# Kernel optimization log

Measured on AMD Instinct MI355X. Metric: run time of the kernel, lower is better.

## Reference

```python
import jax, jax.numpy as jnp
import numpy as np

C = 256   # descriptor_dim
H = 4     # num_heads
D = C // H  # head_dim = 64
B, N = 8, 2048


def _conv1x1(x, w, b):
    # 1x1 Conv1d == per-position linear over channels: x [B,C,N], w [O,C], b [O]
    return jnp.einsum('oc,bcn->bon', w, x) + b[None, :, None]


def setup_inputs() -> dict:
    key = jax.random.key(0)
    ks = jax.random.split(key, 11)
    s = 1.0 / np.sqrt(C)
    return {
        'query': jax.random.normal(ks[0], (B, C, N), dtype=jnp.float32),
        'key':   jax.random.normal(ks[1], (B, C, N), dtype=jnp.float32),
        'value': jax.random.normal(ks[2], (B, C, N), dtype=jnp.float32),
        'wq': jax.random.normal(ks[3], (C, C), dtype=jnp.float32) * s,
        'bq': jax.random.normal(ks[4], (C,), dtype=jnp.float32) * s,
        'wk': jax.random.normal(ks[5], (C, C), dtype=jnp.float32) * s,
        'bk': jax.random.normal(ks[6], (C,), dtype=jnp.float32) * s,
        'wv': jax.random.normal(ks[7], (C, C), dtype=jnp.float32) * s,
        'bv': jax.random.normal(ks[8], (C,), dtype=jnp.float32) * s,
        'wm': jax.random.normal(ks[9], (C, C), dtype=jnp.float32) * s,
        'bm': jax.random.normal(ks[10], (C,), dtype=jnp.float32) * s,
    }


def reference(query, key, value, wq, bq, wk, bk, wv, bv, wm, bm):
    b = query.shape[0]
    # project then view channels as (head_dim, num_heads) -- matches torch .view order
    q = _conv1x1(query, wq, bq).reshape(b, D, H, -1)   # [B,D,H,N]
    k = _conv1x1(key,   wk, bk).reshape(b, D, H, -1)   # [B,D,H,M]
    v = _conv1x1(value, wv, bv).reshape(b, D, H, -1)   # [B,D,H,M]
    scores = jnp.einsum('bdhn,bdhm->bhnm', q, k) / (D ** 0.5)
    probs = jax.nn.softmax(scores, axis=-1)            # [B,H,N,M]
    out = jnp.einsum('bhnm,bdhm->bdhn', probs, v)      # [B,D,H,N]
    out = out.reshape(b, D * H, -1)                    # [B,C,N]
    return _conv1x1(out, wm, bm)
```

## Files before the change

### kernel.cpp

```cpp
#include <hip/hip_runtime.h>
#include <hip/hip_bf16.h>

typedef float f32x4 __attribute__((ext_vector_type(4)));
typedef float f32x16 __attribute__((ext_vector_type(16)));
typedef __bf16 bf16x8 __attribute__((ext_vector_type(8)));
typedef __bf16 bf16x4 __attribute__((ext_vector_type(4)));
typedef unsigned int uint2v __attribute__((ext_vector_type(2)));
typedef unsigned int u32;

constexpr int B_ = 8, C_ = 256, N_ = 2048, H_ = 4, D_ = 64;
constexpr int BH_ = B_ * H_;
constexpr size_t PER_ = (size_t)BH_ * N_ * D_;
constexpr float LOG2E = 1.44269504088896340736f;

static __device__ __forceinline__ float fast_exp2(float x) {
#if __has_builtin(__builtin_amdgcn_exp2f)
  return __builtin_amdgcn_exp2f(x);
#else
  return exp2f(x);
#endif
}

static __device__ __forceinline__ void* swz(void* base, int row, int cb) {
  return (char*)base + row * 128 + (cb ^ ((row & 7) << 4));
}
static __device__ __forceinline__ const void* swz(const void* base, int row, int cb) {
  return (const char*)base + row * 128 + (cb ^ ((row & 7) << 4));
}

static __device__ __forceinline__ void gload16(void* lds, const void* g) {
  __builtin_amdgcn_global_load_lds(
      (const __attribute__((address_space(1))) u32*)g,
      (__attribute__((address_space(3))) u32*)lds, 16, 0, 0);
}

struct W4 {
  const float* s0; const float* s1; const float* s2; const float* s3;
  __bf16* d0; __bf16* d1; __bf16* d2; __bf16* d3;
};

__global__ __launch_bounds__(256) void wcvt_kernel(W4 p) {
  const int m = blockIdx.y;
  const float* src = m == 0 ? p.s0 : m == 1 ? p.s1 : m == 2 ? p.s2 : p.s3;
  __bf16* dst = m == 0 ? p.d0 : m == 1 ? p.d1 : m == 2 ? p.d2 : p.d3;
  const int f = blockIdx.x * 256 + threadIdx.x;
  const int o_blk = f >> 9;
  const int ks = (f >> 6) & 7;
  const int lane = f & 63;
  const int row = o_blk * 16 + (lane & 15);
  const int kbase = ks * 32 + (lane >> 4) * 8;
  bf16x8 v;
  if (m == 3) {
    for (int e = 0; e < 8; e++) {
      const int k = kbase + e;
      const int c = ((k & 63) << 2) | (k >> 6);
      v[e] = (__bf16)src[row * 256 + c];
    }
  } else {
    const int srow = ((row & 63) << 2) | (row >> 6);
    const float* s = src + srow * 256 + kbase;
    float4 a = *(const float4*)s;
    float4 b = *(const float4*)(s + 4);
    v[0] = (__bf16)a.x; v[1] = (__bf16)a.y; v[2] = (__bf16)a.z; v[3] = (__bf16)a.w;
    v[4] = (__bf16)b.x; v[5] = (__bf16)b.y; v[6] = (__bf16)b.z; v[7] = (__bf16)b.w;
  }
  *(bf16x8*)&dst[(size_t)f * 8] = v;
}

__global__ __launch_bounds__(256) void qkv_fused_kernel(
    const float* __restrict__ xq, const float* __restrict__ xk,
    const float* __restrict__ xv, const __bf16* __restrict__ wfq,
    const __bf16* __restrict__ wfk, const __bf16* __restrict__ wfv,
    const float* __restrict__ bq, const float* __restrict__ bk,
    const float* __restrict__ bv, __bf16* __restrict__ oq,
    char* __restrict__ oksw, char* __restrict__ ovsw) {
  __shared__ __bf16 xlds[64][264];

  const int m = blockIdx.x >> 8;
  int inner = blockIdx.x & 255;
  inner = (inner & 7) * 32 + (inner >> 3);
  const int b = inner >> 5, nb = inner & 31;
  const int n0 = nb * 64;

  const float* xf = m == 0 ? xq : m == 1 ? xk : xv;
  const __bf16* wf = m == 0 ? wfq : m == 1 ? wfk : wfv;
  const float* bias = m == 0 ? bq : m == 1 ? bk : bv;
  const float scale = m == 0 ? 0.125f * LOG2E : 1.0f;

  const int t = threadIdx.x;
  {
    const int kl = t & 15;
    const int nl = (t >> 4) * 4;
    const float* src = xf + (size_t)b * C_ * N_ + n0 + nl;
    for (int kp = 0; kp < 8; kp++) {
      const int k = kp * 32 + kl * 2;
      float4 f0 = *(const float4*)(src + (size_t)k * N_);
      float4 f1 = *(const float4*)(src + (size_t)(k + 1) * N_);
      union { __bf16 h[2]; u32 u; } c0, c1, c2, c3;
      c0.h[0] = (__bf16)f0.x; c0.h[1] = (__bf16)f1.x;
      c1.h[0] = (__bf16)f0.y; c1.h[1] = (__bf16)f1.y;
      c2.h[0] = (__bf16)f0.z; c2.h[1] = (__bf16)f1.z;
      c3.h[0] = (__bf16)f0.w; c3.h[1] = (__bf16)f1.w;
      *(u32*)&xlds[nl + 0][k] = c0.u;
      *(u32*)&xlds[nl + 1][k] = c1.u;
      *(u32*)&xlds[nl + 2][k] = c2.u;
      *(u32*)&xlds[nl + 3][k] = c3.u;
    }
  }
  __syncthreads();

  const int lane = t & 63, wvv = t >> 6;
  const int wm = wvv >> 1, wn = wvv & 1;
  const int l15 = lane & 15, lg = lane >> 4;

  f32x4 acc[8][2] = {};

  for (int ks = 0; ks < 8; ks++) {
    bf16x8 bfr[2];
    for (int ni = 0; ni < 2; ni++)
      bfr[ni] = *(const bf16x8*)&xlds[wn * 32 + ni * 16 + l15][ks * 32 + lg * 8];
    for (int mi = 0; mi < 8; mi++) {
      bf16x8 af = *(const bf16x8*)&wf[(((size_t)(wm * 8 + mi) * 8 + ks) * 64 + lane) * 8];
      acc[mi][0] = __builtin_amdgcn_mfma_f32_16x16x32_bf16(af, bfr[0], acc[mi][0], 0, 0, 0);
      acc[mi][1] = __builtin_amdgcn_mfma_f32_16x16x32_bf16(af, bfr[1], acc[mi][1], 0, 0, 0);
    }
  }

  for (int mi = 0; mi < 8; mi++) {
    const int h = wm * 2 + (mi >> 2);
    const int d0 = (mi & 3) * 16 + 4 * lg;
    for (int ni = 0; ni < 2; ni++) {
      const int n = n0 + wn * 32 + ni * 16 + l15;
      const size_t tbase = ((size_t)(b * H_ + h) * (N_ / 64) + (n >> 6)) * 8192;
      if (m == 0) {
        bf16x4 o4;
        for (int r = 0; r < 4; r++)
          o4[r] = (__bf16)((acc[mi][ni][r] + bias[((d0 + r) << 2) | h]) * scale);
        *(bf16x4*)&oq[((size_t)(b * H_ + h) * N_ + n) * D_ + d0] = o4;
      } else if (m == 1) {
        bf16x4 o4;
        for (int r = 0; r < 4; r++)
          o4[r] = (__bf16)(acc[mi][ni][r] + bias[((d0 + r) << 2) | h]);
        *(bf16x4*)swz(oksw + tbase, n & 63, 2 * d0) = o4;
      } else {
        for (int r = 0; r < 4; r++)
          *(__bf16*)swz(ovsw + tbase, d0 + r, 2 * (n & 63)) =
              (__bf16)(acc[mi][ni][r] + bias[((d0 + r) << 2) | h]);
      }
    }
  }
}

template <int COMB>
__global__ __launch_bounds__(256) void final_proj_kernel(
    const __bf16* __restrict__ p0, const __bf16* __restrict__ p1,
    const float* __restrict__ l0, const float* __restrict__ l1,
    const __bf16* __restrict__ wf, const float* __restrict__ bias,
    float* __restrict__ out) {
  const int bid = blockIdx.x;
  const int wid = (bid & 7) * 128 + (bid >> 3);
  const int o_t = wid & 3;
  const int nb = (wid >> 2) & 31;
  const int b = wid >> 7;
  const int o0 = o_t * 64, n0 = nb * 64;
  const int t = threadIdx.x, lane = t & 63;
  const int wvv = t >> 6, wm = wvv >> 1, wn = wvv & 1;
  const int l15 = lane & 15, lg = lane >> 4;
  const int nbase = n0 + wn * 32 + l15;

  float inv[2][4];
  if constexpr (COMB) {
    for (int ni = 0; ni < 2; ni++)
      for (int h = 0; h < 4; h++) {
        const size_t bhn = (size_t)(b * H_ + h) * N_ + nbase + ni * 16;
        inv[ni][h] = 1.f / (l0[bhn] + l1[bhn]);
      }
  }

  f32x4 acc[2][2] = {};

  for (int ks = 0; ks < 8; ks++) {
    bf16x8 af[2];
    for (int mi = 0; mi < 2; mi++)
      af[mi] = *(const bf16x8*)&wf[(((size_t)(o_t * 4 + wm * 2 + mi) * 8 + ks) * 64 + lane) * 8];
    bf16x8 bfr[2];
    const int h = ks >> 1;
    const size_t bh = (size_t)(b * H_ + h);
    const int d0 = (ks & 1) * 32 + lg * 8;
    for (int ni = 0; ni < 2; ni++) {
      const size_t off = (bh * N_ + nbase + ni * 16) * D_ + d0;
      bf16x8 a = *(const bf16x8*)&p0[off];
      if constexpr (COMB) {
        bf16x8 bb = *(const bf16x8*)&p1[off];
        const float iv = inv[ni][h];
        bf16x8 r;
#pragma unroll
        for (int e = 0; e < 8; e++)
          r[e] = (__bf16)(((float)a[e] + (float)bb[e]) * iv);
        bfr[ni] = r;
      } else {
        bfr[ni] = a;
      }
    }
    for (int mi = 0; mi < 2; mi++)
      for (int ni = 0; ni < 2; ni++)
        acc[mi][ni] = __builtin_amdgcn_mfma_f32_16x16x32_bf16(
            af[mi], bfr[ni], acc[mi][ni], 0, 0, 0);
  }

  for (int mi = 0; mi < 2; mi++) {
    for (int r = 0; r < 4; r++) {
      const int och = o0 + wm * 32 + mi * 16 + 4 * lg + r;
      const float bv_ = bias[och];
      for (int ni = 0; ni < 2; ni++) {
        const int n = n0 + wn * 32 + ni * 16 + l15;
        out[((size_t)b * C_ + och) * N_ + n] = acc[mi][ni][r] + bv_;
      }
    }
  }
}

template <int SPLIT>
__global__ __launch_bounds__(512) void attn_kernel(
    const __bf16* __restrict__ qb, const char* __restrict__ kbsw,
    const char* __restrict__ vtsw, __bf16* __restrict__ pO,
    float* __restrict__ lbuf) {
  __shared__ char smem[49152];

  const int t = threadIdx.x, lane = t & 63, wv = t >> 6;
  const int l31 = lane & 31, hi = lane >> 5;

  const int bid = blockIdx.x;
  const int per_xcd = (256 * SPLIT) / 8;
  const int wid = (bid & 7) * per_xcd + (bid >> 3);
  const int bh = wid / (8 * SPLIT);
  const int rem = wid % (8 * SPLIT);
  const int qt = rem & 7;
  const int s = rem >> 3;
  const int qn = qt * 256 + wv * 32;
  constexpr int NT = N_ / SPLIT / 64;
  const int jt0 = s * NT;

  const char* ktiles = kbsw + (size_t)bh * (N_ / 64) * 8192;
  const char* vtiles = vtsw + (size_t)bh * (N_ / 64) * 8192;

  const __bf16* qrow = qb + ((size_t)bh * N_ + qn + l31) * D_;
  bf16x8 qf[4];
#pragma unroll
  for (int i = 0; i < 4; i++) qf[i] = *(const bf16x8*)(qrow + i * 16 + hi * 8);

  auto stage = [&](int jt_g, int bb) {
    gload16(smem + bb * 8192 + t * 16, ktiles + (size_t)jt_g * 8192 + t * 16);
    gload16(smem + 24576 + bb * 8192 + t * 16,
            vtiles + (size_t)jt_g * 8192 + t * 16);
  };

  stage(jt0, 0);
  if (NT > 1) stage(jt0 + 1, 1);
  asm volatile("s_waitcnt vmcnt(2)" ::: "memory");
  __builtin_amdgcn_sched_barrier(0);
  __builtin_amdgcn_s_barrier();
  __builtin_amdgcn_sched_barrier(0);

  f32x16 o0 = {}, o1 = {};
  float la0 = 0.f, la1 = 0.f, la2 = 0.f, la3 = 0.f;
  int cur = 0;

  for (int jt = 0; jt < NT; jt++) {
    if (jt + 2 < NT) {
      int sb = cur + 2; if (sb >= 3) sb -= 3;
      stage(jt0 + jt + 2, sb);
    }
    const char* kc = smem + cur * 8192;
    const char* vc = smem + 24576 + cur * 8192;

    f32x16 s0 = {}, s1 = {};
    __builtin_amdgcn_s_setprio(1);
#pragma unroll
    for (int i = 0; i < 4; i++) {
      bf16x8 kf = *(const bf16x8*)swz(kc, l31, i * 32 + hi * 16);
      s0 = __builtin_amdgcn_mfma_f32_32x32x16_bf16(kf, qf[i], s0, 0, 0, 0);
    }
#pragma unroll
    for (int i = 0; i < 4; i++) {
      bf16x8 kf = *(const bf16x8*)swz(kc, 32 + l31, i * 32 + hi * 16);
      s1 = __builtin_amdgcn_mfma_f32_32x32x16_bf16(kf, qf[i], s1, 0, 0, 0);
    }
    __builtin_amdgcn_s_setprio(0);

#pragma unroll
    for (int sub = 0; sub < 2; sub++) {
      const f32x16 sv = sub ? s1 : s0;
      float pr[16];
#pragma unroll
      for (int r = 0; r < 16; r++) pr[r] = fast_exp2(sv[r]);
      la0 += pr[0] + pr[4] + pr[8] + pr[12];
      la1 += pr[1] + pr[5] + pr[9] + pr[13];
      la2 += pr[2] + pr[6] + pr[10] + pr[14];
      la3 += pr[3] + pr[7] + pr[11] + pr[15];
      unsigned w[8];
#pragma unroll
      for (int g = 0; g < 8; g++) {
        union { __bf16 h[2]; unsigned u; } cv;
        cv.h[0] = (__bf16)pr[2 * g];
        cv.h[1] = (__bf16)pr[2 * g + 1];
        w[g] = cv.u;
      }
      uint2v r0 = __builtin_amdgcn_permlane32_swap(w[0], w[2], false, false);
      uint2v r1 = __builtin_amdgcn_permlane32_swap(w[1], w[3], false, false);
      uint2v r2 = __builtin_amdgcn_permlane32_swap(w[4], w[6], false, false);
      uint2v r3 = __builtin_amdgcn_permlane32_swap(w[5], w[7], false, false);
      union { unsigned u[4]; bf16x8 v; } f0 = {{r0.x, r1.x, r0.y, r1.y}};
      union { unsigned u[4]; bf16x8 v; } f1 = {{r2.x, r3.x, r2.y, r3.y}};
      const int scb = sub * 64;
      __builtin_amdgcn_s_setprio(1);
      {
        bf16x8 vf = *(const bf16x8*)swz(vc, l31, scb + hi * 16);
        o0 = __builtin_amdgcn_mfma_f32_32x32x16_bf16(vf, f0.v, o0, 0, 0, 0);
        vf = *(const bf16x8*)swz(vc, l31, scb + 32 + hi * 16);
        o0 = __builtin_amdgcn_mfma_f32_32x32x16_bf16(vf, f1.v, o0, 0, 0, 0);
        vf = *(const bf16x8*)swz(vc, 32 + l31, scb + hi * 16);
        o1 = __builtin_amdgcn_mfma_f32_32x32x16_bf16(vf, f0.v, o1, 0, 0, 0);
        vf = *(const bf16x8*)swz(vc, 32 + l31, scb + 32 + hi * 16);
        o1 = __builtin_amdgcn_mfma_f32_32x32x16_bf16(vf, f1.v, o1, 0, 0, 0);
      }
      __builtin_amdgcn_s_setprio(0);
    }

    if (jt + 1 < NT) {
      if (jt + 2 < NT) {
        asm volatile("s_waitcnt vmcnt(2)" ::: "memory");
      } else {
        asm volatile("s_waitcnt vmcnt(0)" ::: "memory");
      }
      __builtin_amdgcn_sched_barrier(0);
      __builtin_amdgcn_s_barrier();
      __builtin_amdgcn_sched_barrier(0);
    }
    cur++; if (cur == 3) cur = 0;
  }

  float la = la0 + la1 + la2 + la3;
  la += __shfl_xor(la, 32);
  const float scl = (SPLIT == 1) ? 1.f / la : 1.f;

  if constexpr (SPLIT > 1) {
    if (hi == 0)
      lbuf[(size_t)s * BH_ * N_ + (size_t)bh * N_ + qn + l31] = la;
  }

  __syncthreads();
  char* ep = smem + wv * 4096;
#pragma unroll
  for (int dt = 0; dt < 2; dt++) {
    const f32x16 o = dt ? o1 : o0;
#pragma unroll
    for (int g = 0; g < 4; g++) {
      bf16x4 o4;
#pragma unroll
      for (int j = 0; j < 4; j++) o4[j] = (__bf16)(o[4 * g + j] * scl);
      *(bf16x4*)swz(ep, l31, dt * 64 + 16 * g + 8 * hi) = o4;
    }
  }
  asm volatile("" ::: "memory");
  {
    __bf16* dst = pO + (size_t)s * PER_ + ((size_t)bh * N_ + qn) * D_;
#pragma unroll
    for (int i = 0; i < 4; i++) {
      const int row = i * 8 + (lane >> 3);
      uint4 v = *(const uint4*)swz(ep, row, (lane & 7) * 16);
      *(uint4*)((char*)dst + i * 1024 + lane * 16) = v;
    }
  }
}

extern "C" void kernel_launch(void* const* d_in, const int* in_sizes, int n_in,
                              void* d_out, int out_size, void* d_ws,
                              size_t ws_size, hipStream_t stream) {
  const float* query = (const float*)d_in[0];
  const float* key_ = (const float*)d_in[1];
  const float* value = (const float*)d_in[2];
  const float* wq = (const float*)d_in[3];
  const float* bq = (const float*)d_in[4];
  const float* wk = (const float*)d_in[5];
  const float* bk = (const float*)d_in[6];
  const float* wv = (const float*)d_in[7];
  const float* bv = (const float*)d_in[8];
  const float* wm = (const float*)d_in[9];
  const float* bm = (const float*)d_in[10];

  __bf16* qb = (__bf16*)d_ws;
  char* kbsw = (char*)(qb + PER_);
  char* vtsw = kbsw + PER_ * 2;
  __bf16* p0 = (__bf16*)(vtsw + PER_ * 2);
  __bf16* p1 = p0 + PER_;
  float* lbuf = (float*)(p1 + PER_);
  __bf16* wfq = (__bf16*)(lbuf + 2 * BH_ * N_);
  __bf16* wfk = wfq + 65536;
  __bf16* wfv = wfk + 65536;
  __bf16* wfm = wfv + 65536;

  const size_t need_split = (size_t)((char*)(wfm + 65536) - (char*)d_ws);
  const bool use_split = ws_size >= need_split;

  dim3 blk(256);
  W4 wp{wq, wk, wv, wm, wfq, wfk, wfv, wfm};
  if (!use_split) {
    wfq = p1; wfk = wfq + 65536; wfv = wfk + 65536; wfm = wfv + 65536;
    wp = W4{wq, wk, wv, wm, wfq, wfk, wfv, wfm};
  }
  wcvt_kernel<<<dim3(32, 4), blk, 0, stream>>>(wp);

  qkv_fused_kernel<<<768, blk, 0, stream>>>(query, key_, value, wfq, wfk, wfv,
                                            bq, bk, bv, qb, kbsw, vtsw);
  if (use_split) {
    attn_kernel<2><<<512, dim3(512), 0, stream>>>(qb, kbsw, vtsw, p0, lbuf);
    final_proj_kernel<1><<<1024, blk, 0, stream>>>(
        p0, p1, lbuf, lbuf + BH_ * N_, wfm, bm, (float*)d_out);
  } else {
    attn_kernel<1><<<256, dim3(512), 0, stream>>>(qb, kbsw, vtsw, p0, nullptr);
    final_proj_kernel<0><<<1024, blk, 0, stream>>>(
        p0, p0, nullptr, nullptr, wfm, bm, (float*)d_out);
  }
}
```

Measured before the change: 100.1 us.

## Shrink attention blocks to 256 threads with double-buffered K/V staging

The attention kernel moves from 512-thread blocks with 256 query rows to 256-thread blocks with 128 query rows, doubling the grid and cutting LDS use from 48KB to 32KB. The triple-buffered K/V pipeline, which used explicit vmcnt waits and raw barriers, becomes a simple double buffer with __syncthreads each iteration. The goal is more resident blocks per CU and better latency hiding through occupancy. The cost is that each K/V tile is loaded by twice as many blocks, adding L2 traffic, and the prefetch is only one tile ahead.

```diff
diff --git a/kernel.cpp b/kernel.cpp
--- a/kernel.cpp
+++ b/kernel.cpp
@@ -221,23 +221,23 @@
 }
 
 template <int SPLIT>
-__global__ __launch_bounds__(512) void attn_kernel(
+__global__ __launch_bounds__(256) void attn_kernel(
     const __bf16* __restrict__ qb, const char* __restrict__ kbsw,
     const char* __restrict__ vtsw, __bf16* __restrict__ pO,
     float* __restrict__ lbuf) {
-  __shared__ char smem[49152];
+  __shared__ char smem[32768];
 
   const int t = threadIdx.x, lane = t & 63, wv = t >> 6;
   const int l31 = lane & 31, hi = lane >> 5;
 
   const int bid = blockIdx.x;
-  const int per_xcd = (256 * SPLIT) / 8;
+  const int per_xcd = (512 * SPLIT) / 8;
   const int wid = (bid & 7) * per_xcd + (bid >> 3);
-  const int bh = wid / (8 * SPLIT);
-  const int rem = wid % (8 * SPLIT);
-  const int qt = rem & 7;
-  const int s = rem >> 3;
-  const int qn = qt * 256 + wv * 32;
+  const int bh = wid / (16 * SPLIT);
+  const int rem = wid % (16 * SPLIT);
+  const int qt = rem & 15;
+  const int s = rem >> 4;
+  const int qn = qt * 128 + wv * 32;
   constexpr int NT = N_ / SPLIT / 64;
   const int jt0 = s * NT;
 
@@ -250,29 +250,25 @@
   for (int i = 0; i < 4; i++) qf[i] = *(const bf16x8*)(qrow + i * 16 + hi * 8);
 
   auto stage = [&](int jt_g, int bb) {
-    gload16(smem + bb * 8192 + t * 16, ktiles + (size_t)jt_g * 8192 + t * 16);
-    gload16(smem + 24576 + bb * 8192 + t * 16,
-            vtiles + (size_t)jt_g * 8192 + t * 16);
+    const char* kt = ktiles + (size_t)jt_g * 8192;
+    const char* vt = vtiles + (size_t)jt_g * 8192;
+    gload16(smem + bb * 8192 + t * 16, kt + t * 16);
+    gload16(smem + bb * 8192 + 4096 + t * 16, kt + 4096 + t * 16);
+    gload16(smem + 16384 + bb * 8192 + t * 16, vt + t * 16);
+    gload16(smem + 16384 + bb * 8192 + 4096 + t * 16, vt + 4096 + t * 16);
   };
 
   stage(jt0, 0);
-  if (NT > 1) stage(jt0 + 1, 1);
-  asm volatile("s_waitcnt vmcnt(2)" ::: "memory");
-  __builtin_amdgcn_sched_barrier(0);
-  __builtin_amdgcn_s_barrier();
-  __builtin_amdgcn_sched_barrier(0);
+  __syncthreads();
 
   f32x16 o0 = {}, o1 = {};
   float la0 = 0.f, la1 = 0.f, la2 = 0.f, la3 = 0.f;
   int cur = 0;
 
   for (int jt = 0; jt < NT; jt++) {
-    if (jt + 2 < NT) {
-      int sb = cur + 2; if (sb >= 3) sb -= 3;
-      stage(jt0 + jt + 2, sb);
-    }
+    if (jt + 1 < NT) stage(jt0 + jt + 1, cur ^ 1);
     const char* kc = smem + cur * 8192;
-    const char* vc = smem + 24576 + cur * 8192;
+    const char* vc = smem + 16384 + cur * 8192;
 
     f32x16 s0 = {}, s1 = {};
     __builtin_amdgcn_s_setprio(1);
@@ -327,17 +323,8 @@
       __builtin_amdgcn_s_setprio(0);
     }
 
-    if (jt + 1 < NT) {
-      if (jt + 2 < NT) {
-        asm volatile("s_waitcnt vmcnt(2)" ::: "memory");
-      } else {
-        asm volatile("s_waitcnt vmcnt(0)" ::: "memory");
-      }
-      __builtin_amdgcn_sched_barrier(0);
-      __builtin_amdgcn_s_barrier();
-      __builtin_amdgcn_sched_barrier(0);
-    }
-    cur++; if (cur == 3) cur = 0;
+    __syncthreads();
+    cur ^= 1;
   }
 
   float la = la0 + la1 + la2 + la3;
@@ -349,7 +336,6 @@
       lbuf[(size_t)s * BH_ * N_ + (size_t)bh * N_ + qn + l31] = la;
   }
 
-  __syncthreads();
   char* ep = smem + wv * 4096;
 #pragma unroll
   for (int dt = 0; dt < 2; dt++) {
@@ -414,11 +400,11 @@
   qkv_fused_kernel<<<768, blk, 0, stream>>>(query, key_, value, wfq, wfk, wfv,
                                             bq, bk, bv, qb, kbsw, vtsw);
   if (use_split) {
-    attn_kernel<2><<<512, dim3(512), 0, stream>>>(qb, kbsw, vtsw, p0, lbuf);
+    attn_kernel<2><<<1024, blk, 0, stream>>>(qb, kbsw, vtsw, p0, lbuf);
     final_proj_kernel<1><<<1024, blk, 0, stream>>>(
         p0, p1, lbuf, lbuf + BH_ * N_, wfm, bm, (float*)d_out);
   } else {
-    attn_kernel<1><<<256, dim3(512), 0, stream>>>(qb, kbsw, vtsw, p0, nullptr);
+    attn_kernel<1><<<512, blk, 0, stream>>>(qb, kbsw, vtsw, p0, nullptr);
     final_proj_kernel<0><<<1024, blk, 0, stream>>>(
         p0, p0, nullptr, nullptr, wfm, bm, (float*)d_out);
   }
```

New measurement: 106.5 us. 1.06x slower.
